# Optimization experiments

Measured on AMD Instinct MI355X. Metric: run time of the kernel, lower is better.

Reference implementation:

```python
import jax, jax.numpy as jnp
import numpy as np

N_NODES = 200000
N_EDGES = 3200000


def _gcn_prep(edge_index, n_nodes):
    # Add self loops (PyG GCNConv default) and compute symmetric normalization.
    loops = jnp.arange(n_nodes, dtype=edge_index.dtype)
    src = jnp.concatenate([edge_index[0], loops])
    dst = jnp.concatenate([edge_index[1], loops])
    deg = jax.ops.segment_sum(jnp.ones_like(dst, dtype=jnp.float32), dst,
                              num_segments=n_nodes)
    dinv = jnp.where(deg > 0, jax.lax.rsqrt(deg), 0.0)
    norm = dinv[src] * dinv[dst]  # [E+N]
    return src, dst, norm


def _gcn_conv(x, src, dst, norm, W, b, n_nodes):
    h = x @ W                                   # [N, out]
    msg = h[src] * norm[:, None]                # gather + scale, [E+N, out]
    out = jax.ops.segment_sum(msg, dst, num_segments=n_nodes)  # scatter-add
    return out + b


def setup_inputs() -> dict:
    key = jax.random.key(0)
    k = jax.random.split(key, 4)
    x = jax.random.normal(k[0], (N_NODES, 4), dtype=jnp.float32)
    edge_index = jax.random.randint(k[1], (2, N_EDGES), 0, N_NODES, dtype=jnp.int64)
    W1 = jax.random.normal(k[2], (4, 16), dtype=jnp.float32) * (1.0 / np.sqrt(4))
    b1 = jnp.zeros((16,), dtype=jnp.float32)
    W2 = jax.random.normal(k[3], (16, 1), dtype=jnp.float32) * (1.0 / np.sqrt(16))
    b2 = jnp.zeros((1,), dtype=jnp.float32)
    return {"x": x, "edge_index": edge_index, "W1": W1, "b1": b1,
            "W2": W2, "b2": b2}


def reference(x, edge_index, W1, b1, W2, b2):
    n = x.shape[0]
    src, dst, norm = _gcn_prep(edge_index, n)
    h = _gcn_conv(x, src, dst, norm, W1, b1, n)
    h = jax.nn.relu(h)
    out = _gcn_conv(h, src, dst, norm, W2, b2, n)
    return out
```

## Files before the change

### kernel.cpp

```cpp
#include <hip/hip_runtime.h>


#define BSE   512
#define CH    16384
#define NBW   512
#define SH    9
#define NB    391
#define FCAP  10752
#define BSB   512
#define RSTG4 ((FCAP + 4 * BSB - 1) / (4 * BSB))
#define NOEDGE 0xFFFFFFFFu

typedef unsigned u32x4 __attribute__((ext_vector_type(4)));

__global__ void k_bin(const int* __restrict__ src, const int* __restrict__ dst,
                      int E, unsigned* __restrict__ gcur,
                      unsigned* __restrict__ epack) {
    __shared__ unsigned stage[CH];
    __shared__ unsigned cnt[NB];
    __shared__ unsigned ofs[NB + 1];
    __shared__ unsigned curp[NB];
    __shared__ unsigned gbase[NB];
    __shared__ unsigned wsum[BSE / 64];
    const int b = blockIdx.x, t = threadIdx.x;
    for (int i = t; i < NB; i += BSE) cnt[i] = 0;
    __syncthreads();
    const int lo = b * CH, hi = min(E, lo + CH);
    const int n = hi - lo;
    const int aligned = n & ~3;
    for (int i = 4 * t; i + 3 < n; i += 4 * BSE) {
        int4 d4 = *(const int4*)(dst + lo + i);
        atomicAdd(&cnt[((unsigned)d4.x) >> SH], 1u);
        atomicAdd(&cnt[((unsigned)d4.y) >> SH], 1u);
        atomicAdd(&cnt[((unsigned)d4.z) >> SH], 1u);
        atomicAdd(&cnt[((unsigned)d4.w) >> SH], 1u);
    }
    for (int i = aligned + t; i < n; i += BSE)
        atomicAdd(&cnt[((unsigned)dst[lo + i]) >> SH], 1u);
    __syncthreads();
    const unsigned c = (t < NB) ? cnt[t] : 0u;
    unsigned v = c;
    #pragma unroll
    for (int off = 1; off < 64; off <<= 1) {
        unsigned u = __shfl_up(v, off);
        if ((t & 63) >= off) v += u;
    }
    if ((t & 63) == 63) wsum[t >> 6] = v;
    __syncthreads();
    if (t < BSE / 64) {
        unsigned w = wsum[t];
        #pragma unroll
        for (int off = 1; off < BSE / 64; off <<= 1) {
            unsigned u = __shfl_up(w, off);
            if (t >= off) w += u;
        }
        wsum[t] = w;
    }
    __syncthreads();
    const unsigned incl = v + ((t >> 6) ? wsum[(t >> 6) - 1] : 0u);
    const unsigned excl = incl - c;
    if (t < NB) {
        ofs[t] = excl;
        curp[t] = excl;
        unsigned pad = (c + 15u) & ~15u;
        unsigned o = pad ? atomicAdd(&gcur[t], pad) : 0u;
        gbase[t] = (unsigned)t * FCAP + o;
    }
    if (t == NB - 1) ofs[NB] = incl;
    __syncthreads();
    for (int i = 4 * t; i + 3 < n; i += 4 * BSE) {
        int4 d4 = *(const int4*)(dst + lo + i);
        int4 s4 = *(const int4*)(src + lo + i);
        unsigned k0 = ((unsigned)d4.x) >> SH, k1 = ((unsigned)d4.y) >> SH;
        unsigned k2 = ((unsigned)d4.z) >> SH, k3 = ((unsigned)d4.w) >> SH;
        unsigned p0 = atomicAdd(&curp[k0], 1u);
        unsigned p1 = atomicAdd(&curp[k1], 1u);
        unsigned p2 = atomicAdd(&curp[k2], 1u);
        unsigned p3 = atomicAdd(&curp[k3], 1u);
        stage[p0] = ((unsigned)s4.x << SH) | (((unsigned)d4.x) & (NBW - 1u));
        stage[p1] = ((unsigned)s4.y << SH) | (((unsigned)d4.y) & (NBW - 1u));
        stage[p2] = ((unsigned)s4.z << SH) | (((unsigned)d4.z) & (NBW - 1u));
        stage[p3] = ((unsigned)s4.w << SH) | (((unsigned)d4.w) & (NBW - 1u));
    }
    for (int i = aligned + t; i < n; i += BSE) {
        unsigned d = (unsigned)dst[lo + i];
        unsigned k = d >> SH;
        unsigned pos = atomicAdd(&curp[k], 1u);
        stage[pos] = ((unsigned)src[lo + i] << SH) | (d & (NBW - 1u));
    }
    __syncthreads();
    for (int p0 = 4 * t; p0 < n; p0 += 4 * BSE) {
        unsigned k = 0;
        #pragma unroll
        for (unsigned s = 256; s; s >>= 1) {
            unsigned cand = k + s;
            if (cand <= NB && ofs[cand] <= (unsigned)p0) k = cand;
        }
        #pragma unroll
        for (int j = 0; j < 4; ++j) {
            int p = p0 + j;
            if (p >= n) break;
            while (ofs[k + 1] <= (unsigned)p) ++k;
            unsigned addr = gbase[k] + ((unsigned)p - ofs[k]);
            if (addr < (k + 1u) * FCAP) epack[addr] = stage[p];
        }
    }
    for (int i = t; i < NB; i += BSE) {
        unsigned s = gbase[i] + cnt[i];
        unsigned e = gbase[i] + ((cnt[i] + 15u) & ~15u);
        unsigned kend = ((unsigned)i + 1u) * FCAP;
        if (e > kend) e = kend;
        for (unsigned p = s; p < e; ++p) epack[p] = NOEDGE;
    }
}

__global__ void k_build(unsigned* __restrict__ epack, const unsigned* __restrict__ gcur,
                        const float* __restrict__ x,
                        unsigned* __restrict__ meta,
                        float* __restrict__ x_scaled, int N) {
    __shared__ unsigned stage[FCAP];
    __shared__ unsigned cnt[BSB];
    __shared__ unsigned cur[BSB];
    __shared__ unsigned wsum[BSB / 64];
    __shared__ unsigned s_lenv;
    const int k = blockIdx.x, t = threadIdx.x;
    const unsigned base = (unsigned)k * FCAP;
    const int len = min((int)gcur[k], FCAP);
    const int len4 = len >> 2;
    const u32x4* ep4 = (const u32x4*)(epack + base);
    u32x4 r4[RSTG4];
    #pragma unroll
    for (int j = 0; j < RSTG4; ++j) {
        int i4 = t + j * BSB;
        if (i4 < len4) r4[j] = __builtin_nontemporal_load(ep4 + i4);
        else           r4[j] = (u32x4){NOEDGE, NOEDGE, NOEDGE, NOEDGE};
    }
    cnt[t] = 0;
    __syncthreads();
    #pragma unroll
    for (int j = 0; j < RSTG4; ++j) {
        #pragma unroll
        for (int e = 0; e < 4; ++e) {
            unsigned p = r4[j][e];
            if (p != NOEDGE) atomicAdd(&cnt[p & (NBW - 1u)], 1u);
        }
    }
    __syncthreads();
    const unsigned c  = cnt[t];
    const unsigned cp = (c + 3u) & ~3u;
    unsigned v = cp;
    #pragma unroll
    for (int off = 1; off < 64; off <<= 1) {
        unsigned u = __shfl_up(v, off);
        if ((t & 63) >= off) v += u;
    }
    if ((t & 63) == 63) wsum[t >> 6] = v;
    __syncthreads();
    if (t < BSB / 64) {
        unsigned w = wsum[t];
        #pragma unroll
        for (int off = 1; off < BSB / 64; off <<= 1) {
            unsigned u = __shfl_up(w, off);
            if (t >= off) w += u;
        }
        wsum[t] = w;
    }
    __syncthreads();
    const unsigned incl = v + ((t >> 6) ? wsum[(t >> 6) - 1] : 0u);
    const unsigned excl = incl - cp;
    cur[t] = excl;
    if (t == BSB - 1) s_lenv = incl;
    const int node = k * NBW + t;
    if (node < N) {
        meta[node] = excl | (c << 14);
        float di = rsqrtf((float)(c + 1u));
        float4 xv = ((const float4*)x)[node];
        ((float4*)x_scaled)[node] = make_float4(xv.x * di, xv.y * di, xv.z * di, xv.w * di);
    }
    __syncthreads();
    #pragma unroll
    for (int j = 0; j < RSTG4; ++j) {
        #pragma unroll
        for (int e = 0; e < 4; ++e) {
            unsigned p = r4[j][e];
            if (p != NOEDGE) {
                unsigned pos = atomicAdd(&cur[p & (NBW - 1u)], 1u);
                if (pos < FCAP) stage[pos] = p >> SH;
            }
        }
    }
    __syncthreads();
    const int lenv = min((int)s_lenv, FCAP);
    for (int i = 4 * t; i < lenv; i += 4 * BSB)
        *(int4*)(epack + base + i) = *(const int4*)&stage[i];
}

__global__ void k_agg1(const unsigned* __restrict__ esorted, const unsigned* __restrict__ meta,
                       const float* __restrict__ x_scaled,
                       const float* __restrict__ W1, const float* __restrict__ b1,
                       const float* __restrict__ W2,
                       float* __restrict__ z_scaled, int N) {
    int node = blockIdx.x * blockDim.x + threadIdx.x;
    if (node >= N) return;
    unsigned m = meta[node];
    unsigned c = m >> 14;
    unsigned lo = (unsigned)(node >> SH) * FCAP + (m & 16383u);
    unsigned hi = lo + c;
    float di = rsqrtf((float)(c + 1u));
    const float4* xs4 = (const float4*)x_scaled;
    float4 a0 = xs4[node];
    float4 a1 = make_float4(0.f, 0.f, 0.f, 0.f);
    float4 a2 = make_float4(0.f, 0.f, 0.f, 0.f);
    float4 a3 = make_float4(0.f, 0.f, 0.f, 0.f);
    unsigned i = lo;
    for (; i + 7 < hi; i += 8) {
        u32x4 e0 = *(const u32x4*)(esorted + i);
        u32x4 e1 = *(const u32x4*)(esorted + i + 4);
        float4 v0 = xs4[e0[0]], v1 = xs4[e0[1]], v2 = xs4[e0[2]], v3 = xs4[e0[3]];
        float4 v4 = xs4[e1[0]], v5 = xs4[e1[1]], v6 = xs4[e1[2]], v7 = xs4[e1[3]];
        a0.x += v0.x; a0.y += v0.y; a0.z += v0.z; a0.w += v0.w;
        a1.x += v1.x; a1.y += v1.y; a1.z += v1.z; a1.w += v1.w;
        a2.x += v2.x; a2.y += v2.y; a2.z += v2.z; a2.w += v2.w;
        a3.x += v3.x; a3.y += v3.y; a3.z += v3.z; a3.w += v3.w;
        a0.x += v4.x; a0.y += v4.y; a0.z += v4.z; a0.w += v4.w;
        a1.x += v5.x; a1.y += v5.y; a1.z += v5.z; a1.w += v5.w;
        a2.x += v6.x; a2.y += v6.y; a2.z += v6.z; a2.w += v6.w;
        a3.x += v7.x; a3.y += v7.y; a3.z += v7.z; a3.w += v7.w;
    }
    if (i + 3 < hi) {
        u32x4 e0 = *(const u32x4*)(esorted + i);
        float4 v0 = xs4[e0[0]], v1 = xs4[e0[1]], v2 = xs4[e0[2]], v3 = xs4[e0[3]];
        a0.x += v0.x; a0.y += v0.y; a0.z += v0.z; a0.w += v0.w;
        a1.x += v1.x; a1.y += v1.y; a1.z += v1.z; a1.w += v1.w;
        a2.x += v2.x; a2.y += v2.y; a2.z += v2.z; a2.w += v2.w;
        a3.x += v3.x; a3.y += v3.y; a3.z += v3.z; a3.w += v3.w;
        i += 4;
    }
    for (; i < hi; ++i) {
        float4 v = xs4[esorted[i]];
        a0.x += v.x; a0.y += v.y; a0.z += v.z; a0.w += v.w;
    }
    float p0 = di * (a0.x + a1.x + a2.x + a3.x);
    float p1 = di * (a0.y + a1.y + a2.y + a3.y);
    float p2 = di * (a0.z + a1.z + a2.z + a3.z);
    float p3 = di * (a0.w + a1.w + a2.w + a3.w);
    float z = 0.0f;
    #pragma unroll
    for (int cc = 0; cc < 16; ++cc) {
        float h1 = p0 * W1[0 * 16 + cc] + p1 * W1[1 * 16 + cc]
                 + p2 * W1[2 * 16 + cc] + p3 * W1[3 * 16 + cc] + b1[cc];
        h1 = fmaxf(h1, 0.0f);
        z += h1 * W2[cc];
    }
    z_scaled[node] = z * di;
}

__global__ void k_agg2(const unsigned* __restrict__ esorted, const unsigned* __restrict__ meta,
                       const float* __restrict__ z_scaled,
                       const float* __restrict__ b2, float* __restrict__ out, int N) {
    int node = blockIdx.x * blockDim.x + threadIdx.x;
    if (node >= N) return;
    unsigned m = meta[node];
    unsigned c = m >> 14;
    unsigned lo = (unsigned)(node >> SH) * FCAP + (m & 16383u);
    unsigned hi = lo + c;
    float di = rsqrtf((float)(c + 1u));
    float a0 = z_scaled[node], a1 = 0.f, a2 = 0.f, a3 = 0.f;
    unsigned i = lo;
    for (; i + 7 < hi; i += 8) {
        u32x4 e0 = __builtin_nontemporal_load((const u32x4*)(esorted + i));
        u32x4 e1 = __builtin_nontemporal_load((const u32x4*)(esorted + i + 4));
        a0 += z_scaled[e0[0]]; a1 += z_scaled[e0[1]];
        a2 += z_scaled[e0[2]]; a3 += z_scaled[e0[3]];
        a0 += z_scaled[e1[0]]; a1 += z_scaled[e1[1]];
        a2 += z_scaled[e1[2]]; a3 += z_scaled[e1[3]];
    }
    if (i + 3 < hi) {
        u32x4 e0 = __builtin_nontemporal_load((const u32x4*)(esorted + i));
        a0 += z_scaled[e0[0]]; a1 += z_scaled[e0[1]];
        a2 += z_scaled[e0[2]]; a3 += z_scaled[e0[3]];
        i += 4;
    }
    for (; i < hi; ++i) a0 += z_scaled[esorted[i]];
    out[node] = di * (a0 + a1 + a2 + a3) + b2[0];
}

extern "C" void kernel_launch(void* const* d_in, const int* in_sizes, int n_in,
                              void* d_out, int out_size, void* d_ws, size_t ws_size,
                              hipStream_t stream) {
    const float* x  = (const float*)d_in[0];
    const int*   ei = (const int*)d_in[1];
    const float* W1 = (const float*)d_in[2];
    const float* b1 = (const float*)d_in[3];
    const float* W2 = (const float*)d_in[4];
    const float* b2 = (const float*)d_in[5];

    const int N = in_sizes[0] / 4;
    const int E = in_sizes[1] / 2;
    const int* src = ei;
    const int* dst = ei + E;
    const int NA = (E + CH - 1) / CH;

    char* ws = (char*)d_ws;
    unsigned* gcur     = (unsigned*)ws;  ws += 4096;
    unsigned* epack    = (unsigned*)ws;  ws += (size_t)NB * FCAP * 4;
    unsigned* meta     = (unsigned*)ws;  ws += (size_t)N * 4;
    float*    x_scaled = (float*)ws;     ws += (size_t)N * 4 * 4;
    float*    z_scaled = (float*)ws;     ws += (size_t)N * 4;
    float* out = (float*)d_out;

    hipMemsetAsync(gcur, 0, NB * sizeof(unsigned), stream);
    k_bin  <<<NA, BSE, 0, stream>>>(src, dst, E, gcur, epack);
    k_build<<<NB, BSB, 0, stream>>>(epack, gcur, x, meta, x_scaled, N);
    k_agg1 <<<(N + 255) / 256, 256, 0, stream>>>(epack, meta, x_scaled,
                                                 W1, b1, W2, z_scaled, N);
    k_agg2 <<<(N + 255) / 256, 256, 0, stream>>>(epack, meta, z_scaled, b2, out, N);
}
```

Before: 166.4 us.

## Reorder nodes by in-degree within each bin to balance aggregation warps

In k_build, each node's in-degree is histogrammed within its 512-node bin, and a 16-bit permutation is written that sorts the nodes by degree. The aggregation kernels read this permutation, so each wavefront handles nodes with similar edge counts, which is meant to cut divergence and idle lanes in the gather loops. Separately, the nontemporal loads on the edge lists are replaced with ordinary cached loads. The cost is an extra permutation array, some LDS atomics in k_build, and gathers that now hit memory in a less sequential order.

```diff
diff --git a/kernel.cpp b/kernel.cpp
--- a/kernel.cpp
+++ b/kernel.cpp
@@ -116,12 +116,13 @@
 
 __global__ void k_build(unsigned* __restrict__ epack, const unsigned* __restrict__ gcur,
                         const float* __restrict__ x,
-                        unsigned* __restrict__ meta,
+                        unsigned* __restrict__ meta, unsigned short* __restrict__ perm16,
                         float* __restrict__ x_scaled, int N) {
     __shared__ unsigned stage[FCAP];
     __shared__ unsigned cnt[BSB];
     __shared__ unsigned cur[BSB];
     __shared__ unsigned wsum[BSB / 64];
+    __shared__ unsigned hist[64];
     __shared__ unsigned s_lenv;
     const int k = blockIdx.x, t = threadIdx.x;
     const unsigned base = (unsigned)k * FCAP;
@@ -132,10 +133,11 @@
     #pragma unroll
     for (int j = 0; j < RSTG4; ++j) {
         int i4 = t + j * BSB;
-        if (i4 < len4) r4[j] = __builtin_nontemporal_load(ep4 + i4);
+        if (i4 < len4) r4[j] = ep4[i4];
         else           r4[j] = (u32x4){NOEDGE, NOEDGE, NOEDGE, NOEDGE};
     }
     cnt[t] = 0;
+    if (t < 64) hist[t] = 0;
     __syncthreads();
     #pragma unroll
     for (int j = 0; j < RSTG4; ++j) {
@@ -147,6 +149,8 @@
     }
     __syncthreads();
     const unsigned c  = cnt[t];
+    const unsigned dbin = min(c, 63u);
+    atomicAdd(&hist[dbin], 1u);
     const unsigned cp = (c + 3u) & ~3u;
     unsigned v = cp;
     #pragma unroll
@@ -164,12 +168,23 @@
             if (t >= off) w += u;
         }
         wsum[t] = w;
+    }
+    if (t < 64) {
+        unsigned h = hist[t], s = h;
+        #pragma unroll
+        for (int off = 1; off < 64; off <<= 1) {
+            unsigned u = __shfl_up(s, off);
+            if (t >= off) s += u;
+        }
+        hist[t] = s - h;
     }
     __syncthreads();
     const unsigned incl = v + ((t >> 6) ? wsum[(t >> 6) - 1] : 0u);
     const unsigned excl = incl - cp;
     cur[t] = excl;
     if (t == BSB - 1) s_lenv = incl;
+    const unsigned rank = atomicAdd(&hist[dbin], 1u);
+    perm16[(unsigned)k * NBW + rank] = (unsigned short)t;
     const int node = k * NBW + t;
     if (node < N) {
         meta[node] = excl | (c << 14);
@@ -196,15 +211,19 @@
 }
 
 __global__ void k_agg1(const unsigned* __restrict__ esorted, const unsigned* __restrict__ meta,
+                       const unsigned short* __restrict__ perm16,
                        const float* __restrict__ x_scaled,
                        const float* __restrict__ W1, const float* __restrict__ b1,
                        const float* __restrict__ W2,
                        float* __restrict__ z_scaled, int N) {
-    int node = blockIdx.x * blockDim.x + threadIdx.x;
+    int r = blockIdx.x * blockDim.x + threadIdx.x;
+    if (r >= NB * NBW) return;
+    int b = r >> SH;
+    int node = (b << SH) + perm16[r];
     if (node >= N) return;
     unsigned m = meta[node];
     unsigned c = m >> 14;
-    unsigned lo = (unsigned)(node >> SH) * FCAP + (m & 16383u);
+    unsigned lo = (unsigned)b * FCAP + (m & 16383u);
     unsigned hi = lo + c;
     float di = rsqrtf((float)(c + 1u));
     const float4* xs4 = (const float4*)x_scaled;
@@ -256,27 +275,31 @@
 }
 
 __global__ void k_agg2(const unsigned* __restrict__ esorted, const unsigned* __restrict__ meta,
+                       const unsigned short* __restrict__ perm16,
                        const float* __restrict__ z_scaled,
                        const float* __restrict__ b2, float* __restrict__ out, int N) {
-    int node = blockIdx.x * blockDim.x + threadIdx.x;
+    int r = blockIdx.x * blockDim.x + threadIdx.x;
+    if (r >= NB * NBW) return;
+    int b = r >> SH;
+    int node = (b << SH) + perm16[r];
     if (node >= N) return;
     unsigned m = meta[node];
     unsigned c = m >> 14;
-    unsigned lo = (unsigned)(node >> SH) * FCAP + (m & 16383u);
+    unsigned lo = (unsigned)b * FCAP + (m & 16383u);
     unsigned hi = lo + c;
     float di = rsqrtf((float)(c + 1u));
     float a0 = z_scaled[node], a1 = 0.f, a2 = 0.f, a3 = 0.f;
     unsigned i = lo;
     for (; i + 7 < hi; i += 8) {
-        u32x4 e0 = __builtin_nontemporal_load((const u32x4*)(esorted + i));
-        u32x4 e1 = __builtin_nontemporal_load((const u32x4*)(esorted + i + 4));
+        u32x4 e0 = *(const u32x4*)(esorted + i);
+        u32x4 e1 = *(const u32x4*)(esorted + i + 4);
         a0 += z_scaled[e0[0]]; a1 += z_scaled[e0[1]];
         a2 += z_scaled[e0[2]]; a3 += z_scaled[e0[3]];
         a0 += z_scaled[e1[0]]; a1 += z_scaled[e1[1]];
         a2 += z_scaled[e1[2]]; a3 += z_scaled[e1[3]];
     }
     if (i + 3 < hi) {
-        u32x4 e0 = __builtin_nontemporal_load((const u32x4*)(esorted + i));
+        u32x4 e0 = *(const u32x4*)(esorted + i);
         a0 += z_scaled[e0[0]]; a1 += z_scaled[e0[1]];
         a2 += z_scaled[e0[2]]; a3 += z_scaled[e0[3]];
         i += 4;
@@ -302,17 +325,20 @@
     const int NA = (E + CH - 1) / CH;
 
     char* ws = (char*)d_ws;
-    unsigned* gcur     = (unsigned*)ws;  ws += 4096;
-    unsigned* epack    = (unsigned*)ws;  ws += (size_t)NB * FCAP * 4;
-    unsigned* meta     = (unsigned*)ws;  ws += (size_t)N * 4;
-    float*    x_scaled = (float*)ws;     ws += (size_t)N * 4 * 4;
-    float*    z_scaled = (float*)ws;     ws += (size_t)N * 4;
+    unsigned* gcur       = (unsigned*)ws;       ws += 4096;
+    unsigned* epack      = (unsigned*)ws;       ws += (size_t)NB * FCAP * 4;
+    unsigned* meta       = (unsigned*)ws;       ws += (size_t)N * 4;
+    unsigned short* perm = (unsigned short*)ws; ws += (size_t)NB * NBW * 2;
+    float*    x_scaled   = (float*)ws;          ws += (size_t)N * 4 * 4;
+    float*    z_scaled   = (float*)ws;          ws += (size_t)N * 4;
     float* out = (float*)d_out;
 
+    const int NR = NB * NBW;
     hipMemsetAsync(gcur, 0, NB * sizeof(unsigned), stream);
     k_bin  <<<NA, BSE, 0, stream>>>(src, dst, E, gcur, epack);
-    k_build<<<NB, BSB, 0, stream>>>(epack, gcur, x, meta, x_scaled, N);
-    k_agg1 <<<(N + 255) / 256, 256, 0, stream>>>(epack, meta, x_scaled,
-                                                 W1, b1, W2, z_scaled, N);
-    k_agg2 <<<(N + 255) / 256, 256, 0, stream>>>(epack, meta, z_scaled, b2, out, N);
-}
+    k_build<<<NB, BSB, 0, stream>>>(epack, gcur, x, meta, perm, x_scaled, N);
+    k_agg1 <<<(NR + 255) / 256, 256, 0, stream>>>(epack, meta, perm, x_scaled,
+                                                  W1, b1, W2, z_scaled, N);
+    k_agg2 <<<(NR + 255) / 256, 256, 0, stream>>>(epack, meta, perm, z_scaled,
+                                                  b2, out, N);
+}
```

Result: slower. 173.1 us (+4.1%).
